# Kernel optimization log

Hardware: AMD Instinct MI355X
Metric: run time of the kernel (lower is better)

## Reference

```python
import jax, jax.numpy as jnp
import numpy as np

BETA = 0.5
N = 4096

def setup_inputs() -> dict:
    key = jax.random.key(0)
    k1, k2, k3 = jax.random.split(key, 3)
    A = jax.random.uniform(k1, (N, N), dtype=jnp.float32)
    h = jax.random.normal(k2, (N, N), dtype=jnp.float32)
    W = jax.random.normal(k3, (N, N), dtype=jnp.float32) * (1.0 / np.sqrt(N))
    return {"A": A, "h": h, "W": W}

def reference(A, h, W):
    # degrees from original A (before self-loops); D = diag(deg) + I is diagonal,
    # so torch.inverse(D) == elementwise reciprocal 1/(deg+1)
    deg = jnp.sum(A, axis=1)                       # [N]
    inv_d = 1.0 / (deg + 1.0)                      # [N]
    A_I = A + jnp.eye(A.shape[0], dtype=A.dtype)   # A += I
    # A_st = (A+I) @ diag(inv_d): scale columns
    A_st = A_I * inv_d[None, :]                    # [N,N]
    # A_st_11 = A_st @ h is dead code in the original (never used) -> skipped
    temp = BETA * h + (1.0 - BETA) * A_st          # [N,N]
    return temp @ W                                # [N,N]
```

## Files before the change

kernel.cpp:

```cpp
#include <hip/hip_runtime.h>
#include <hip/hip_bf16.h>

typedef unsigned short u16;
typedef unsigned int u32;
typedef __attribute__((ext_vector_type(8))) short bf16x8;
typedef __attribute__((ext_vector_type(4))) short s16x4;
typedef __attribute__((ext_vector_type(4))) float f32x4;

#define NN 4096

__device__ __forceinline__ u16 f2bf(float f) {
    union { float f; u32 u; } v; v.f = f;
    u32 r = v.u + 0x7fffu + ((v.u >> 16) & 1u);
    return (u16)(r >> 16);
}

__global__ void rowsum_kernel(const float* __restrict__ A, float* __restrict__ invd) {
    const int row = blockIdx.x;
    const float4* a4 = reinterpret_cast<const float4*>(A + (size_t)row * NN);
    float s = 0.f;
    #pragma unroll
    for (int i = 0; i < 4; ++i) {
        float4 v = a4[threadIdx.x + i * 256];
        s += v.x + v.y + v.z + v.w;
    }
    #pragma unroll
    for (int off = 32; off > 0; off >>= 1) s += __shfl_down(s, off, 64);
    __shared__ float ws[4];
    if ((threadIdx.x & 63) == 0) ws[threadIdx.x >> 6] = s;
    __syncthreads();
    if (threadIdx.x == 0) {
        float t = ws[0] + ws[1] + ws[2] + ws[3];
        invd[row] = 1.0f / (t + 1.0f);
    }
}

__global__ void make_temp_kernel(const float* __restrict__ A, const float* __restrict__ h,
                                 const float* __restrict__ invd, u16* __restrict__ T) {
    const size_t g = ((size_t)blockIdx.x * 256 + threadIdx.x) * 8;
    const int row = (int)(g >> 12);
    const int col = (int)(g & 4095);
    const float4* a4 = reinterpret_cast<const float4*>(A + g);
    const float4* h4 = reinterpret_cast<const float4*>(h + g);
    const float4* d4 = reinterpret_cast<const float4*>(invd + col);
    float4 a0 = a4[0], a1 = a4[1];
    float4 h0 = h4[0], h1 = h4[1];
    float4 dd0 = d4[0], dd1 = d4[1];
    float av[8] = {a0.x,a0.y,a0.z,a0.w,a1.x,a1.y,a1.z,a1.w};
    float hv[8] = {h0.x,h0.y,h0.z,h0.w,h1.x,h1.y,h1.z,h1.w};
    float dv[8] = {dd0.x,dd0.y,dd0.z,dd0.w,dd1.x,dd1.y,dd1.z,dd1.w};
    bf16x8 o;
    #pragma unroll
    for (int j = 0; j < 8; ++j) {
        float aa = av[j] + ((col + j == row) ? 1.0f : 0.0f);
        float t = 0.5f * hv[j] + 0.5f * aa * dv[j];
        o[j] = (short)f2bf(t);
    }
    *reinterpret_cast<bf16x8*>(T + g) = o;
}

__global__ void transposeW_kernel(const float* __restrict__ W, u16* __restrict__ Wt) {
    __shared__ float tile[64][65];
    const int nt = blockIdx.x & 63;
    const int kt = blockIdx.x >> 6;
    const int k0 = kt * 64, n0 = nt * 64;
    const int tr = threadIdx.x >> 4;
    const int tc = (threadIdx.x & 15) * 4;
    #pragma unroll
    for (int rr = 0; rr < 64; rr += 16) {
        float4 v = *reinterpret_cast<const float4*>(&W[(size_t)(k0 + tr + rr) * NN + n0 + tc]);
        tile[tr + rr][tc + 0] = v.x;
        tile[tr + rr][tc + 1] = v.y;
        tile[tr + rr][tc + 2] = v.z;
        tile[tr + rr][tc + 3] = v.w;
    }
    __syncthreads();
    #pragma unroll
    for (int rr = 0; rr < 64; rr += 16) {
        const int n = tr + rr;
        s16x4 o;
        #pragma unroll
        for (int j = 0; j < 4; ++j) o[j] = (short)f2bf(tile[tc + j][n]);
        *reinterpret_cast<s16x4*>(&Wt[(size_t)(n0 + n) * NN + k0 + tc]) = o;
    }
}


#define GLD16(g, l) __builtin_amdgcn_global_load_lds( \
    (const __attribute__((address_space(1))) void*)(g), \
    (__attribute__((address_space(3))) void*)(l), 16, 0, 0)

__global__ __launch_bounds__(512, 2) void gemm_kernel(
    const u16* __restrict__ Atl,
    const u16* __restrict__ Btl,
    float* __restrict__ C)
{
    __shared__ u16 S[4][2][8192];

    const int tid  = threadIdx.x;
    const int wid  = tid >> 6;
    const int lane = tid & 63;
    const int llo  = lane & 15;
    const int lhi  = lane >> 4;
    const int wr   = wid >> 2;
    const int wc   = wid & 3;

    const int swz = ((int)blockIdx.x & 7) * 32 + ((int)blockIdx.x >> 3);
    const int bm = swz >> 4, bn = swz & 15;
    const int tileRow = bm * 256, tileCol = bn * 256;

    const int r0 = tid >> 2;
    const int kc = (((tid & 3) ^ ((r0 >> 1) & 3)) << 3);
    const u16* gA0 = Atl + (size_t)(tileRow + r0) * NN + kc;
    const u16* gA1 = gA0 + (size_t)128 * NN;
    const u16* gB0 = Btl + (size_t)(tileCol + r0) * NN + kc;
    const u16* gB1 = gB0 + (size_t)128 * NN;

    int offA[8], offB[4];
    #pragma unroll
    for (int m = 0; m < 8; ++m) {
        const int row = wr * 128 + m * 16 + llo;
        offA[m] = row * 32 + ((lhi ^ ((row >> 1) & 3)) << 3);
    }
    #pragma unroll
    for (int n = 0; n < 4; ++n) {
        const int row = wc * 64 + n * 16 + llo;
        offB[n] = row * 32 + ((lhi ^ ((row >> 1) & 3)) << 3);
    }

    f32x4 acc[8][4];
    #pragma unroll
    for (int m = 0; m < 8; ++m)
        #pragma unroll
        for (int n = 0; n < 4; ++n)
            acc[m][n] = (f32x4){0.f, 0.f, 0.f, 0.f};

    #pragma unroll
    for (int p = 0; p < 3; ++p) {
        GLD16(gA0 + p * 32, &S[p][0][wid * 512]);
        GLD16(gA1 + p * 32, &S[p][0][4096 + wid * 512]);
        GLD16(gB0 + p * 32, &S[p][1][wid * 512]);
        GLD16(gB1 + p * 32, &S[p][1][4096 + wid * 512]);
    }
    gA0 += 96; gA1 += 96; gB0 += 96; gB1 += 96;
    asm volatile("s_waitcnt vmcnt(8)" ::: "memory");
    __builtin_amdgcn_s_barrier();
    asm volatile("" ::: "memory");

    #pragma unroll 1
    for (int t = 0; t < 128; ++t) {
        if (t < 125) {
            const int b3 = (t + 3) & 3;
            GLD16(gA0, &S[b3][0][wid * 512]);
            GLD16(gA1, &S[b3][0][4096 + wid * 512]);
            GLD16(gB0, &S[b3][1][wid * 512]);
            GLD16(gB1, &S[b3][1][4096 + wid * 512]);
            gA0 += 32; gA1 += 32; gB0 += 32; gB1 += 32;
        }
        __builtin_amdgcn_sched_barrier(0);

        const int b = t & 3;
        const u16* sA = &S[b][0][0];
        const u16* sB = &S[b][1][0];
        bf16x8 af[8], bv[4];
        #pragma unroll
        for (int m = 0; m < 8; ++m)
            af[m] = *reinterpret_cast<const bf16x8*>(sA + offA[m]);
        #pragma unroll
        for (int n = 0; n < 4; ++n)
            bv[n] = *reinterpret_cast<const bf16x8*>(sB + offB[n]);

        __builtin_amdgcn_s_setprio(1);
        #pragma unroll
        for (int m = 0; m < 8; ++m)
            #pragma unroll
            for (int n = 0; n < 4; ++n)
                acc[m][n] = __builtin_amdgcn_mfma_f32_16x16x32_bf16(
                    af[m], bv[n], acc[m][n], 0, 0, 0);
        __builtin_amdgcn_s_setprio(0);

        if (t < 125)       asm volatile("s_waitcnt vmcnt(8)" ::: "memory");
        else if (t == 125) asm volatile("s_waitcnt vmcnt(4)" ::: "memory");
        else if (t == 126) asm volatile("s_waitcnt vmcnt(0)" ::: "memory");
        if (t < 127) {
            __builtin_amdgcn_s_barrier();
            asm volatile("" ::: "memory");
        }
    }

    #pragma unroll
    for (int m = 0; m < 8; ++m) {
        #pragma unroll
        for (int n = 0; n < 4; ++n) {
            const size_t rbase = (size_t)(tileRow + wr * 128 + m * 16 + lhi * 4) * NN
                               + tileCol + wc * 64 + n * 16 + llo;
            #pragma unroll
            for (int j = 0; j < 4; ++j)
                C[rbase + (size_t)j * NN] = acc[m][n][j];
        }
    }
}

extern "C" void kernel_launch(void* const* d_in, const int* in_sizes, int n_in,
                              void* d_out, int out_size, void* d_ws, size_t ws_size,
                              hipStream_t stream) {
    const float* A = (const float*)d_in[0];
    const float* h = (const float*)d_in[1];
    const float* W = (const float*)d_in[2];
    float* out = (float*)d_out;

    float* invd = (float*)d_ws;
    u16* temp = (u16*)((char*)d_ws + 16384);
    u16* wt   = temp + (size_t)NN * NN;

    rowsum_kernel<<<NN, 256, 0, stream>>>(A, invd);
    make_temp_kernel<<<(NN * (size_t)NN) / (256 * 8), 256, 0, stream>>>(A, h, invd, temp);
    transposeW_kernel<<<(NN / 64) * (NN / 64), 256, 0, stream>>>(W, wt);
    gemm_kernel<<<256, 512, 0, stream>>>(temp, wt, out);
}
```

Before: 176.8 us.

## Restructure GEMM main loop into two-role ping-pong with triple-buffered LDS

The 8 waves of the GEMM block are split into two roles that alternate phases. One half reads fragments from LDS while the other half issues MFMAs, with two barriers per k-step keeping them staggered. The intent is to overlap LDS reads with matrix-core work across waves instead of serialising them within each wave. LDS staging drops from four buffers to three, with prefetch two steps ahead. The extra barrier per step and the shallower prefetch could expose more global-load latency.

```diff
diff --git a/kernel.cpp b/kernel.cpp
--- a/kernel.cpp
+++ b/kernel.cpp
@@ -95,7 +95,7 @@
     const u16* __restrict__ Btl,
     float* __restrict__ C)
 {
-    __shared__ u16 S[4][2][8192];
+    __shared__ u16 S[3][2][8192];
 
     const int tid  = threadIdx.x;
     const int wid  = tid >> 6;
@@ -104,6 +104,7 @@
     const int lhi  = lane >> 4;
     const int wr   = wid >> 2;
     const int wc   = wid & 3;
+    const bool role1 = (wr != 0);
 
     const int swz = ((int)blockIdx.x & 7) * 32 + ((int)blockIdx.x >> 3);
     const int bm = swz >> 4, bn = swz & 15;
@@ -111,10 +112,17 @@
 
     const int r0 = tid >> 2;
     const int kc = (((tid & 3) ^ ((r0 >> 1) & 3)) << 3);
+    const size_t R128 = (size_t)128 * NN;
     const u16* gA0 = Atl + (size_t)(tileRow + r0) * NN + kc;
-    const u16* gA1 = gA0 + (size_t)128 * NN;
+    const u16* gA1 = gA0 + R128;
     const u16* gB0 = Btl + (size_t)(tileCol + r0) * NN + kc;
-    const u16* gB1 = gB0 + (size_t)128 * NN;
+    const u16* gB1 = gB0 + R128;
+
+    #define STAGE(WB, KOFF) do { \
+        GLD16(gA0 + (KOFF), &S[WB][0][tid * 8]); \
+        GLD16(gA1 + (KOFF), &S[WB][0][4096 + tid * 8]); \
+        GLD16(gB0 + (KOFF), &S[WB][1][tid * 8]); \
+        GLD16(gB1 + (KOFF), &S[WB][1][4096 + tid * 8]); } while (0)
 
     int offA[8], offB[4];
     #pragma unroll
@@ -135,58 +143,65 @@
         for (int n = 0; n < 4; ++n)
             acc[m][n] = (f32x4){0.f, 0.f, 0.f, 0.f};
 
-    #pragma unroll
-    for (int p = 0; p < 3; ++p) {
-        GLD16(gA0 + p * 32, &S[p][0][wid * 512]);
-        GLD16(gA1 + p * 32, &S[p][0][4096 + wid * 512]);
-        GLD16(gB0 + p * 32, &S[p][1][wid * 512]);
-        GLD16(gB1 + p * 32, &S[p][1][4096 + wid * 512]);
-    }
-    gA0 += 96; gA1 += 96; gB0 += 96; gB1 += 96;
-    asm volatile("s_waitcnt vmcnt(8)" ::: "memory");
+    bf16x8 af[8], bv[4];
+
+    #define READF(BI) do { \
+        const u16* sA = &S[BI][0][0]; \
+        const u16* sB = &S[BI][1][0]; \
+        _Pragma("unroll") \
+        for (int m = 0; m < 8; ++m) af[m] = *reinterpret_cast<const bf16x8*>(sA + offA[m]); \
+        _Pragma("unroll") \
+        for (int n = 0; n < 4; ++n) bv[n] = *reinterpret_cast<const bf16x8*>(sB + offB[n]); \
+    } while (0)
+
+    #define MFMACL() do { \
+        __builtin_amdgcn_s_setprio(1); \
+        _Pragma("unroll") \
+        for (int m = 0; m < 8; ++m) \
+            _Pragma("unroll") \
+            for (int n = 0; n < 4; ++n) \
+                acc[m][n] = __builtin_amdgcn_mfma_f32_16x16x32_bf16(af[m], bv[n], acc[m][n], 0, 0, 0); \
+        __builtin_amdgcn_s_setprio(0); \
+    } while (0)
+
+    STAGE(0, 0);
+    STAGE(1, 32);
+    asm volatile("s_waitcnt vmcnt(4)" ::: "memory");
     __builtin_amdgcn_s_barrier();
     asm volatile("" ::: "memory");
 
+    int bi = 0;
+    int bw = 2;
+
     #pragma unroll 1
-    for (int t = 0; t < 128; ++t) {
-        if (t < 125) {
-            const int b3 = (t + 3) & 3;
-            GLD16(gA0, &S[b3][0][wid * 512]);
-            GLD16(gA1, &S[b3][0][4096 + wid * 512]);
-            GLD16(gB0, &S[b3][1][wid * 512]);
-            GLD16(gB1, &S[b3][1][4096 + wid * 512]);
-            gA0 += 32; gA1 += 32; gB0 += 32; gB1 += 32;
+    for (int s = 0; s < 128; ++s) {
+        if (s <= 125) STAGE(bw, (s + 2) * 32);
+        __builtin_amdgcn_sched_barrier(0);
+        if (!role1) {
+            READF(bi);
+        } else if (s > 0) {
+            MFMACL();
         }
-        __builtin_amdgcn_sched_barrier(0);
-
-        const int b = t & 3;
-        const u16* sA = &S[b][0][0];
-        const u16* sB = &S[b][1][0];
-        bf16x8 af[8], bv[4];
-        #pragma unroll
-        for (int m = 0; m < 8; ++m)
-            af[m] = *reinterpret_cast<const bf16x8*>(sA + offA[m]);
-        #pragma unroll
-        for (int n = 0; n < 4; ++n)
-            bv[n] = *reinterpret_cast<const bf16x8*>(sB + offB[n]);
-
-        __builtin_amdgcn_s_setprio(1);
-        #pragma unroll
-        for (int m = 0; m < 8; ++m)
-            #pragma unroll
-            for (int n = 0; n < 4; ++n)
-                acc[m][n] = __builtin_amdgcn_mfma_f32_16x16x32_bf16(
-                    af[m], bv[n], acc[m][n], 0, 0, 0);
-        __builtin_amdgcn_s_setprio(0);
-
-        if (t < 125)       asm volatile("s_waitcnt vmcnt(8)" ::: "memory");
-        else if (t == 125) asm volatile("s_waitcnt vmcnt(4)" ::: "memory");
-        else if (t == 126) asm volatile("s_waitcnt vmcnt(0)" ::: "memory");
-        if (t < 127) {
-            __builtin_amdgcn_s_barrier();
-            asm volatile("" ::: "memory");
+        __builtin_amdgcn_s_barrier();
+        asm volatile("" ::: "memory");
+
+        if (!role1) {
+            MFMACL();
+        } else {
+            READF(bi);
         }
-    }
+        if (s <= 125)      asm volatile("s_waitcnt vmcnt(4)" ::: "memory");
+        else if (s == 126) asm volatile("s_waitcnt vmcnt(0)" ::: "memory");
+        __builtin_amdgcn_s_barrier();
+        asm volatile("" ::: "memory");
+
+        bi = (bi == 2) ? 0 : bi + 1;
+        bw = (bw == 2) ? 0 : bw + 1;
+    }
+    if (role1) MFMACL();
+    #undef STAGE
+    #undef READF
+    #undef MFMACL
 
     #pragma unroll
     for (int m = 0; m < 8; ++m) {
```

Result: no change. 178.6 us (+1.0%).
